# Kernel optimization log

Hardware: AMD Instinct MI355X
Metric: run time of the kernel (lower is better)

The kernel has to match this reference:

```python
import jax, jax.numpy as jnp
import numpy as np

NEG = -1000000000.0


def setup_inputs() -> dict:
    key = jax.random.key(0)
    k1, k2, k3, k4, k5 = jax.random.split(key, 5)
    B, T, D, Q = 8, 2048, 1024, 128
    x = jax.random.normal(k1, (B, T, D), dtype=jnp.float32)
    attn_mask = jax.random.randint(k2, (B, T), 0, 2).astype(jnp.bool_)
    s = 1.0 / np.sqrt(D)
    Wq = jax.random.normal(k3, (Q, D), dtype=jnp.float32) * s
    Wk = jax.random.normal(k4, (Q, D), dtype=jnp.float32) * s
    Wv = jax.random.normal(k5, (Q, D), dtype=jnp.float32) * s
    return {"x": x, "attn_mask": attn_mask, "Wq": Wq, "Wk": Wk, "Wv": Wv}


def reference(x, attn_mask, Wq, Wk, Wv):
    # x: (B,T,D); W*: (Q,D) torch Linear weights (y = x @ W.T)
    q = jnp.einsum('btd,qd->btq', x, Wq)
    k = jnp.einsum('btd,qd->btq', x, Wk)
    v = jnp.einsum('btd,qd->btq', x, Wv)
    logits = jnp.einsum('btq,bsq->bts', q, k)  # (B,T,T), no 1/sqrt(d) scaling (matches source)
    m = attn_mask[:, None, :]  # (B,1,T) broadcasts over query dim, == repeat(1,T,1)
    logits = jnp.where(m, logits, NEG)
    A = jax.nn.softmax(logits, axis=-1)
    A = jnp.where(m, A, 0.0)
    return jnp.einsum('bts,bsq->btq', A, v)
```

## Files before the change

kernel.cpp:

```cpp
#include <hip/hip_runtime.h>
#include <hip/hip_bf16.h>
#include <hip/hip_fp16.h>

typedef _Float16 half8 __attribute__((ext_vector_type(8)));
typedef _Float16 half4v __attribute__((ext_vector_type(4)));
typedef float float4v __attribute__((ext_vector_type(4)));

#define MFMA_F16(a, b, c) __builtin_amdgcn_mfma_f32_16x16x32_f16((a), (b), (c), 0, 0, 0)

#define GLDS16(gp, lp) \
    __builtin_amdgcn_global_load_lds((const __attribute__((address_space(1))) unsigned int*)(gp), \
                                     (__attribute__((address_space(3))) unsigned int*)(lp), 16, 0, 0)

#define BATCH 8
#define SEQ   2048
#define DIM   1024
#define QD    128
#define BT    (BATCH * SEQ)
#define NSPLIT 4
#define KSPAN (SEQ / NSPLIT)

__device__ __forceinline__ float dpp_max16(float x) {
    int v;
    v = __builtin_amdgcn_update_dpp(0, __float_as_int(x), 0xB1, 0xF, 0xF, false);
    x = fmaxf(x, __int_as_float(v));
    v = __builtin_amdgcn_update_dpp(0, __float_as_int(x), 0x4E, 0xF, 0xF, false);
    x = fmaxf(x, __int_as_float(v));
    v = __builtin_amdgcn_update_dpp(0, __float_as_int(x), 0x141, 0xF, 0xF, false);
    x = fmaxf(x, __int_as_float(v));
    v = __builtin_amdgcn_update_dpp(0, __float_as_int(x), 0x140, 0xF, 0xF, false);
    x = fmaxf(x, __int_as_float(v));
    return x;
}

__global__ __launch_bounds__(256) void cvt_x_kernel(const float* __restrict__ s,
                                                    _Float16* __restrict__ d) {
    int i = blockIdx.x * 256 + threadIdx.x;
    float4 f = ((const float4*)s)[i];
    half4v h = {(_Float16)f.x, (_Float16)f.y, (_Float16)f.z, (_Float16)f.w};
    ((half4v*)d)[i] = h;
}

__global__ __launch_bounds__(256) void cvt_w_kernel(const float* __restrict__ Wq,
                                                    const float* __restrict__ Wk,
                                                    const float* __restrict__ Wv,
                                                    _Float16* __restrict__ Wh) {
    const float* src = (blockIdx.y == 0) ? Wq : ((blockIdx.y == 1) ? Wk : Wv);
    int i = blockIdx.x * 256 + threadIdx.x;
    float4 f = ((const float4*)src)[i];
    half4v h = {(_Float16)f.x, (_Float16)f.y, (_Float16)f.z, (_Float16)f.w};
    ((half4v*)(Wh + (size_t)blockIdx.y * QD * DIM))[i] = h;
}

__global__ __launch_bounds__(256, 3) void proj_kernel(
    const _Float16* __restrict__ xh,
    const _Float16* __restrict__ Wh,
    _Float16* __restrict__ q_out,
    _Float16* __restrict__ k_out,
    _Float16* __restrict__ vt_out)
{
    __shared__ _Float16 As[64 * 64];
    __shared__ _Float16 Bs[128 * 64];

    const int tid  = threadIdx.x;
    const int lane = tid & 63;
    const int wave = tid >> 6;
    const int quad = lane >> 4;
    const int l15  = lane & 15;
    const int wr   = wave >> 1;
    const int wc   = wave & 1;

    const int which = blockIdx.y;
    const _Float16* W = Wh + (size_t)which * QD * DIM;
    const int row0 = blockIdx.x * 64;

    float4v acc[2][4];
#pragma unroll
    for (int rf = 0; rf < 2; rf++)
#pragma unroll
        for (int n = 0; n < 4; n++)
            acc[rf][n] = (float4v){0.f, 0.f, 0.f, 0.f};

    for (int kk = 0; kk < DIM; kk += 64) {
        __syncthreads();
#pragma unroll
        for (int c = 0; c < 2; c++) {
            int ci = wave * 128 + c * 64 + lane;
            int r  = ci >> 3;
            int g  = (ci & 7) ^ (r & 7);
            GLDS16(xh + (size_t)(row0 + r) * DIM + kk + g * 8, &As[(wave * 128 + c * 64) * 8]);
        }
#pragma unroll
        for (int c = 0; c < 4; c++) {
            int ci = wave * 256 + c * 64 + lane;
            int r  = ci >> 3;
            int g  = (ci & 7) ^ (r & 7);
            GLDS16(W + (size_t)r * DIM + kk + g * 8, &Bs[(wave * 256 + c * 64) * 8]);
        }
        __syncthreads();

        half8 af[2][2], bf[4][2];
#pragma unroll
        for (int rf = 0; rf < 2; rf++)
#pragma unroll
            for (int kc = 0; kc < 2; kc++) {
                int r = wr * 32 + rf * 16 + l15;
                int g = (kc * 4 + quad) ^ (r & 7);
                af[rf][kc] = *(const half8*)&As[r * 64 + g * 8];
            }
#pragma unroll
        for (int n = 0; n < 4; n++)
#pragma unroll
            for (int kc = 0; kc < 2; kc++) {
                int r = wc * 64 + n * 16 + l15;
                int g = (kc * 4 + quad) ^ (r & 7);
                bf[n][kc] = *(const half8*)&Bs[r * 64 + g * 8];
            }
#pragma unroll
        for (int kc = 0; kc < 2; kc++)
#pragma unroll
            for (int rf = 0; rf < 2; rf++)
#pragma unroll
                for (int n = 0; n < 4; n++)
                    acc[rf][n] = MFMA_F16(af[rf][kc], bf[n][kc], acc[rf][n]);
    }

    if (which == 2) {
#pragma unroll
        for (int rf = 0; rf < 2; rf++) {
            int grow0 = row0 + wr * 32 + rf * 16 + quad * 4;
            int b  = grow0 >> 11;
            int t0 = grow0 & 2047;
#pragma unroll
            for (int n = 0; n < 4; n++) {
                int col = wc * 64 + n * 16 + l15;
                half4v h;
#pragma unroll
                for (int r = 0; r < 4; r++) h[r] = (_Float16)acc[rf][n][r];
                *(half4v*)&vt_out[((size_t)(b * QD + col)) * SEQ + t0] = h;
            }
        }
    } else {
        _Float16* out = (which == 0) ? q_out : k_out;
#pragma unroll
        for (int rf = 0; rf < 2; rf++) {
            int grow0 = row0 + wr * 32 + rf * 16 + quad * 4;
#pragma unroll
            for (int n = 0; n < 4; n++) {
                int col = wc * 64 + n * 16 + l15;
#pragma unroll
                for (int r = 0; r < 4; r++)
                    out[(size_t)(grow0 + r) * QD + col] = (_Float16)acc[rf][n][r];
            }
        }
    }
}

__global__ __launch_bounds__(256, 2) void attn_kernel(
    const _Float16* __restrict__ q,
    const _Float16* __restrict__ k,
    const _Float16* __restrict__ vt,
    const int* __restrict__ mask,
    _Float16* __restrict__ Op,
    float2* __restrict__ ml)
{
    __shared__ _Float16 Ks[64 * 128];
    __shared__ _Float16 Vs[128 * 64];
    __shared__ _Float16 Ps[4 * 32 * 64];
    __shared__ int Ms[64];

    const int tid  = threadIdx.x;
    const int lane = tid & 63;
    const int wave = tid >> 6;
    const int quad = lane >> 4;
    const int l15  = lane & 15;

    const int b  = blockIdx.y;
    const int z  = blockIdx.z;
    const int rowbase = blockIdx.x * 128 + wave * 32;

    half8 qf[2][4];
#pragma unroll
    for (int rf = 0; rf < 2; rf++) {
        const _Float16* qrow = q + ((size_t)(b * SEQ + rowbase + rf * 16 + l15)) * QD + quad * 8;
#pragma unroll
        for (int kc = 0; kc < 4; kc++)
            qf[rf][kc] = *(const half8*)(qrow + kc * 32);
    }

    const half8 onesv = {(_Float16)1, (_Float16)1, (_Float16)1, (_Float16)1,
                         (_Float16)1, (_Float16)1, (_Float16)1, (_Float16)1};

    float4v oacc[2][8];
#pragma unroll
    for (int rf = 0; rf < 2; rf++)
#pragma unroll
        for (int n = 0; n < 8; n++)
            oacc[rf][n] = (float4v){0.f, 0.f, 0.f, 0.f};
    float4v lacc[2] = {(float4v){0.f, 0.f, 0.f, 0.f}, (float4v){0.f, 0.f, 0.f, 0.f}};
    float mrow[2][4];
#pragma unroll
    for (int rf = 0; rf < 2; rf++)
#pragma unroll
        for (int r = 0; r < 4; r++) mrow[rf][r] = -1e30f;

    _Float16* Pw = &Ps[wave * 32 * 64];

    for (int sb = z * KSPAN; sb < z * KSPAN + KSPAN; sb += 64) {
        __syncthreads();
#pragma unroll
        for (int c = 0; c < 4; c++) {
            int ci = wave * 256 + c * 64 + lane;
            int r  = ci >> 4;
            int gs = ci & 15;
            int g  = (gs & 8) | ((gs ^ r) & 7);
            GLDS16(k + ((size_t)(b * SEQ + sb + r)) * QD + g * 8, &Ks[(wave * 256 + c * 64) * 8]);
        }
#pragma unroll
        for (int c = 0; c < 4; c++) {
            int ci = wave * 256 + c * 64 + lane;
            int r  = ci >> 3;
            int g  = ((ci & 7) ^ r) & 7;
            GLDS16(vt + ((size_t)(b * QD + r)) * SEQ + sb + g * 8, &Vs[(wave * 256 + c * 64) * 8]);
        }
        if (tid < 64) Ms[tid] = mask[b * SEQ + sb + tid];
        __syncthreads();

        float4v sacc[2][4];
#pragma unroll
        for (int rf = 0; rf < 2; rf++)
#pragma unroll
            for (int j = 0; j < 4; j++)
                sacc[rf][j] = (float4v){0.f, 0.f, 0.f, 0.f};
#pragma unroll
        for (int kc = 0; kc < 4; kc++) {
            half8 kf[4];
#pragma unroll
            for (int j = 0; j < 4; j++) {
                int r  = j * 16 + l15;
                int g  = kc * 4 + quad;
                int gs = (g & 8) | ((g ^ r) & 7);
                kf[j] = *(const half8*)&Ks[r * 128 + gs * 8];
            }
#pragma unroll
            for (int rf = 0; rf < 2; rf++)
#pragma unroll
                for (int j = 0; j < 4; j++)
                    sacc[rf][j] = MFMA_F16(qf[rf][kc], kf[j], sacc[rf][j]);
        }

        float alpha[2][4];
#pragma unroll
        for (int rf = 0; rf < 2; rf++) {
            float rmax[4] = {-1e30f, -1e30f, -1e30f, -1e30f};
#pragma unroll
            for (int j = 0; j < 4; j++) {
                bool m_ok = (Ms[j * 16 + l15] != 0);
#pragma unroll
                for (int r = 0; r < 4; r++) {
                    float s = m_ok ? sacc[rf][j][r] : -1e30f;
                    sacc[rf][j][r] = s;
                    rmax[r] = fmaxf(rmax[r], s);
                }
            }
#pragma unroll
            for (int r = 0; r < 4; r++) {
                float rm = dpp_max16(rmax[r]);
                float mnew = fmaxf(mrow[rf][r], rm);
                alpha[rf][r] = __expf(mrow[rf][r] - mnew);
                mrow[rf][r] = mnew;
            }
        }

#pragma unroll
        for (int rf = 0; rf < 2; rf++)
#pragma unroll
            for (int j = 0; j < 4; j++) {
                int col = j * 16 + l15;
                int gc  = col >> 3;
#pragma unroll
                for (int r = 0; r < 4; r++) {
                    int m  = rf * 16 + quad * 4 + r;
                    int gs = (gc ^ m) & 7;
                    float s = sacc[rf][j][r];
                    float p = (s > -1e29f) ? __expf(s - mrow[rf][r]) : 0.f;
                    Pw[m * 64 + gs * 8 + (col & 7)] = (_Float16)p;
                }
            }

#pragma unroll
        for (int rf = 0; rf < 2; rf++) {
#pragma unroll
            for (int n = 0; n < 8; n++)
#pragma unroll
                for (int r = 0; r < 4; r++)
                    oacc[rf][n][r] *= alpha[rf][r];
#pragma unroll
            for (int r = 0; r < 4; r++) lacc[rf][r] *= alpha[rf][r];
        }

#pragma unroll
        for (int kc = 0; kc < 2; kc++) {
            half8 pf[2];
#pragma unroll
            for (int rf = 0; rf < 2; rf++) {
                int m  = rf * 16 + l15;
                int gs = ((kc * 4 + quad) ^ m) & 7;
                pf[rf] = *(const half8*)&Pw[m * 64 + gs * 8];
            }
#pragma unroll
            for (int n = 0; n < 8; n++) {
                int r  = n * 16 + l15;
                int gs = ((kc * 4 + quad) ^ r) & 7;
                half8 vf = *(const half8*)&Vs[r * 64 + gs * 8];
#pragma unroll
                for (int rf = 0; rf < 2; rf++)
                    oacc[rf][n] = MFMA_F16(pf[rf], vf, oacc[rf][n]);
            }
#pragma unroll
            for (int rf = 0; rf < 2; rf++)
                lacc[rf] = MFMA_F16(pf[rf], onesv, lacc[rf]);
        }
    }

    _Float16* Oz = Op + (size_t)z * BT * QD;
#pragma unroll
    for (int rf = 0; rf < 2; rf++) {
#pragma unroll
        for (int n = 0; n < 8; n++) {
            int col = n * 16 + l15;
#pragma unroll
            for (int r = 0; r < 4; r++) {
                int row = rowbase + rf * 16 + quad * 4 + r;
                Oz[((size_t)(b * SEQ + row)) * QD + col] = (_Float16)oacc[rf][n][r];
            }
        }
        if (l15 == 0) {
#pragma unroll
            for (int r = 0; r < 4; r++) {
                int row = rowbase + rf * 16 + quad * 4 + r;
                ml[(size_t)z * BT + b * SEQ + row] = make_float2(mrow[rf][r], lacc[rf][r]);
            }
        }
    }
}

__global__ __launch_bounds__(256) void merge_kernel(
    const _Float16* __restrict__ Op,
    const float2* __restrict__ ml,
    float* __restrict__ out)
{
    int gid = blockIdx.x * 256 + threadIdx.x;
    int row = gid >> 4;
    int c8  = (gid & 15) * 8;

    float2 a[NSPLIT];
    float m = -3.0e38f;
#pragma unroll
    for (int s = 0; s < NSPLIT; s++) { a[s] = ml[(size_t)s * BT + row]; m = fmaxf(m, a[s].x); }
    float sc[NSPLIT];
    float denom = 0.f;
#pragma unroll
    for (int s = 0; s < NSPLIT; s++) { sc[s] = __expf(a[s].x - m); denom += sc[s] * a[s].y; }
    float inv = (denom > 0.f) ? (1.0f / denom) : 0.f;

    float acc[8] = {0, 0, 0, 0, 0, 0, 0, 0};
#pragma unroll
    for (int s = 0; s < NSPLIT; s++) {
        half8 o = *(const half8*)&Op[(size_t)s * BT * QD + (size_t)row * QD + c8];
#pragma unroll
        for (int e = 0; e < 8; e++) acc[e] += (float)o[e] * sc[s];
    }
    float4 lo = make_float4(acc[0] * inv, acc[1] * inv, acc[2] * inv, acc[3] * inv);
    float4 hi = make_float4(acc[4] * inv, acc[5] * inv, acc[6] * inv, acc[7] * inv);
    *(float4*)&out[(size_t)row * QD + c8] = lo;
    *(float4*)&out[(size_t)row * QD + c8 + 4] = hi;
}

extern "C" void kernel_launch(void* const* d_in, const int* in_sizes, int n_in,
                              void* d_out, int out_size, void* d_ws, size_t ws_size,
                              hipStream_t stream) {
    const float* x    = (const float*)d_in[0];
    const int*   mask = (const int*)d_in[1];
    const float* Wq   = (const float*)d_in[2];
    const float* Wk   = (const float*)d_in[3];
    const float* Wv   = (const float*)d_in[4];
    float* out = (float*)d_out;

    char* p = (char*)d_ws;
    _Float16* xh  = (_Float16*)p; p += (size_t)BT * DIM * 2;
    _Float16* Wh  = (_Float16*)p; p += (size_t)3 * QD * DIM * 2;
    _Float16* qb  = (_Float16*)p; p += (size_t)BT * QD * 2;
    _Float16* kb  = (_Float16*)p; p += (size_t)BT * QD * 2;
    _Float16* vtb = (_Float16*)p; p += (size_t)BT * QD * 2;
    _Float16* Op  = (_Float16*)p; p += (size_t)NSPLIT * BT * QD * 2;
    float2*   ml  = (float2*)p;

    cvt_x_kernel<<<dim3(BT * DIM / 4 / 256), 256, 0, stream>>>(x, xh);
    cvt_w_kernel<<<dim3(QD * DIM / 4 / 256, 3), 256, 0, stream>>>(Wq, Wk, Wv, Wh);
    proj_kernel<<<dim3(BT / 64, 3), 256, 0, stream>>>(xh, Wh, qb, kb, vtb);
    attn_kernel<<<dim3(SEQ / 128, BATCH, NSPLIT), 256, 0, stream>>>(qb, kb, vtb, mask, Op, ml);
    merge_kernel<<<dim3(BT * 16 / 256), 256, 0, stream>>>(Op, ml, out);
}
```

Measured before the change: 163.4 us.

## Fuse convert kernels, widen projection K-tile, alias P onto K buffer, double splits

Merges the x and weight fp16 conversion kernels into one launch. Doubles the projection K-step to 128, halving the number of barrier-separated iterations. In attention, the P scratch now reuses the K tile's shared memory, with an added barrier, which cuts LDS use so launch bounds can request 4 blocks per SM. NSPLIT goes from 4 to 8 for more parallelism, at the cost of a larger partial-output buffer, more merge traffic and higher register pressure.

```diff
diff --git a/kernel.cpp b/kernel.cpp
--- a/kernel.cpp
+++ b/kernel.cpp
@@ -17,7 +17,7 @@
 #define DIM   1024
 #define QD    128
 #define BT    (BATCH * SEQ)
-#define NSPLIT 4
+#define NSPLIT 8
 #define KSPAN (SEQ / NSPLIT)
 
 __device__ __forceinline__ float dpp_max16(float x) {
@@ -33,23 +33,31 @@
     return x;
 }
 
-__global__ __launch_bounds__(256) void cvt_x_kernel(const float* __restrict__ s,
-                                                    _Float16* __restrict__ d) {
+#define XN4 (BT * DIM / 4)
+#define WN4 (3 * QD * DIM / 4)
+
+__global__ __launch_bounds__(256) void cvt_kernel(
+    const float* __restrict__ x,
+    const float* __restrict__ Wq,
+    const float* __restrict__ Wk,
+    const float* __restrict__ Wv,
+    _Float16* __restrict__ xh,
+    _Float16* __restrict__ Wh)
+{
     int i = blockIdx.x * 256 + threadIdx.x;
-    float4 f = ((const float4*)s)[i];
-    half4v h = {(_Float16)f.x, (_Float16)f.y, (_Float16)f.z, (_Float16)f.w};
-    ((half4v*)d)[i] = h;
-}
-
-__global__ __launch_bounds__(256) void cvt_w_kernel(const float* __restrict__ Wq,
-                                                    const float* __restrict__ Wk,
-                                                    const float* __restrict__ Wv,
-                                                    _Float16* __restrict__ Wh) {
-    const float* src = (blockIdx.y == 0) ? Wq : ((blockIdx.y == 1) ? Wk : Wv);
-    int i = blockIdx.x * 256 + threadIdx.x;
-    float4 f = ((const float4*)src)[i];
-    half4v h = {(_Float16)f.x, (_Float16)f.y, (_Float16)f.z, (_Float16)f.w};
-    ((half4v*)(Wh + (size_t)blockIdx.y * QD * DIM))[i] = h;
+    if (i < XN4) {
+        float4 f = ((const float4*)x)[i];
+        half4v h = {(_Float16)f.x, (_Float16)f.y, (_Float16)f.z, (_Float16)f.w};
+        ((half4v*)xh)[i] = h;
+    } else {
+        int j = i - XN4;
+        int which = j >> 15;
+        int o = j & 32767;
+        const float* src = (which == 0) ? Wq : ((which == 1) ? Wk : Wv);
+        float4 f = ((const float4*)src)[o];
+        half4v h = {(_Float16)f.x, (_Float16)f.y, (_Float16)f.z, (_Float16)f.w};
+        ((half4v*)Wh)[j] = h;
+    }
 }
 
 __global__ __launch_bounds__(256, 3) void proj_kernel(
@@ -59,8 +67,8 @@
     _Float16* __restrict__ k_out,
     _Float16* __restrict__ vt_out)
 {
-    __shared__ _Float16 As[64 * 64];
-    __shared__ _Float16 Bs[128 * 64];
+    __shared__ _Float16 As[64 * 128];
+    __shared__ _Float16 Bs[128 * 128];
 
     const int tid  = threadIdx.x;
     const int lane = tid & 63;
@@ -81,48 +89,49 @@
         for (int n = 0; n < 4; n++)
             acc[rf][n] = (float4v){0.f, 0.f, 0.f, 0.f};
 
-    for (int kk = 0; kk < DIM; kk += 64) {
+    for (int kk = 0; kk < DIM; kk += 128) {
         __syncthreads();
-#pragma unroll
-        for (int c = 0; c < 2; c++) {
-            int ci = wave * 128 + c * 64 + lane;
-            int r  = ci >> 3;
-            int g  = (ci & 7) ^ (r & 7);
-            GLDS16(xh + (size_t)(row0 + r) * DIM + kk + g * 8, &As[(wave * 128 + c * 64) * 8]);
-        }
 #pragma unroll
         for (int c = 0; c < 4; c++) {
             int ci = wave * 256 + c * 64 + lane;
-            int r  = ci >> 3;
-            int g  = (ci & 7) ^ (r & 7);
-            GLDS16(W + (size_t)r * DIM + kk + g * 8, &Bs[(wave * 256 + c * 64) * 8]);
+            int r  = ci >> 4;
+            int gs = ci & 15;
+            int g  = (gs & 8) | ((gs ^ r) & 7);
+            GLDS16(xh + (size_t)(row0 + r) * DIM + kk + g * 8, &As[(wave * 256 + c * 64) * 8]);
+        }
+#pragma unroll
+        for (int c = 0; c < 8; c++) {
+            int ci = wave * 512 + c * 64 + lane;
+            int r  = ci >> 4;
+            int gs = ci & 15;
+            int g  = (gs & 8) | ((gs ^ r) & 7);
+            GLDS16(W + (size_t)r * DIM + kk + g * 8, &Bs[(wave * 512 + c * 64) * 8]);
         }
         __syncthreads();
 
-        half8 af[2][2], bf[4][2];
-#pragma unroll
-        for (int rf = 0; rf < 2; rf++)
-#pragma unroll
-            for (int kc = 0; kc < 2; kc++) {
+#pragma unroll
+        for (int kc = 0; kc < 4; kc++) {
+            half8 af[2], bf[4];
+#pragma unroll
+            for (int rf = 0; rf < 2; rf++) {
                 int r = wr * 32 + rf * 16 + l15;
-                int g = (kc * 4 + quad) ^ (r & 7);
-                af[rf][kc] = *(const half8*)&As[r * 64 + g * 8];
-            }
-#pragma unroll
-        for (int n = 0; n < 4; n++)
-#pragma unroll
-            for (int kc = 0; kc < 2; kc++) {
+                int g = kc * 4 + quad;
+                int gp = (g & 8) | ((g ^ r) & 7);
+                af[rf] = *(const half8*)&As[r * 128 + gp * 8];
+            }
+#pragma unroll
+            for (int n = 0; n < 4; n++) {
                 int r = wc * 64 + n * 16 + l15;
-                int g = (kc * 4 + quad) ^ (r & 7);
-                bf[n][kc] = *(const half8*)&Bs[r * 64 + g * 8];
-            }
-#pragma unroll
-        for (int kc = 0; kc < 2; kc++)
+                int g = kc * 4 + quad;
+                int gp = (g & 8) | ((g ^ r) & 7);
+                bf[n] = *(const half8*)&Bs[r * 128 + gp * 8];
+            }
 #pragma unroll
             for (int rf = 0; rf < 2; rf++)
 #pragma unroll
                 for (int n = 0; n < 4; n++)
-                    acc[rf][n] = MFMA_F16(af[rf][kc], bf[n][kc], acc[rf][n]);
+                    acc[rf][n] = MFMA_F16(af[rf], bf[n], acc[rf][n]);
+        }
     }
 
     if (which == 2) {
@@ -156,7 +165,7 @@
     }
 }
 
-__global__ __launch_bounds__(256, 2) void attn_kernel(
+__global__ __launch_bounds__(256, 4) void attn_kernel(
     const _Float16* __restrict__ q,
     const _Float16* __restrict__ k,
     const _Float16* __restrict__ vt,
@@ -164,9 +173,8 @@
     _Float16* __restrict__ Op,
     float2* __restrict__ ml)
 {
-    __shared__ _Float16 Ks[64 * 128];
+    __shared__ _Float16 KPs[64 * 128];
     __shared__ _Float16 Vs[128 * 64];
-    __shared__ _Float16 Ps[4 * 32 * 64];
     __shared__ int Ms[64];
 
     const int tid  = threadIdx.x;
@@ -204,7 +212,7 @@
 #pragma unroll
         for (int r = 0; r < 4; r++) mrow[rf][r] = -1e30f;
 
-    _Float16* Pw = &Ps[wave * 32 * 64];
+    _Float16* Pw = &KPs[wave * 32 * 64];
 
     for (int sb = z * KSPAN; sb < z * KSPAN + KSPAN; sb += 64) {
         __syncthreads();
@@ -214,7 +222,7 @@
             int r  = ci >> 4;
             int gs = ci & 15;
             int g  = (gs & 8) | ((gs ^ r) & 7);
-            GLDS16(k + ((size_t)(b * SEQ + sb + r)) * QD + g * 8, &Ks[(wave * 256 + c * 64) * 8]);
+            GLDS16(k + ((size_t)(b * SEQ + sb + r)) * QD + g * 8, &KPs[(wave * 256 + c * 64) * 8]);
         }
 #pragma unroll
         for (int c = 0; c < 4; c++) {
@@ -240,7 +248,7 @@
                 int r  = j * 16 + l15;
                 int g  = kc * 4 + quad;
                 int gs = (g & 8) | ((g ^ r) & 7);
-                kf[j] = *(const half8*)&Ks[r * 128 + gs * 8];
+                kf[j] = *(const half8*)&KPs[r * 128 + gs * 8];
             }
 #pragma unroll
             for (int rf = 0; rf < 2; rf++)
@@ -271,6 +279,19 @@
                 mrow[rf][r] = mnew;
             }
         }
+
+#pragma unroll
+        for (int rf = 0; rf < 2; rf++) {
+#pragma unroll
+            for (int n = 0; n < 8; n++)
+#pragma unroll
+                for (int r = 0; r < 4; r++)
+                    oacc[rf][n][r] *= alpha[rf][r];
+#pragma unroll
+            for (int r = 0; r < 4; r++) lacc[rf][r] *= alpha[rf][r];
+        }
+
+        __syncthreads();
 
 #pragma unroll
         for (int rf = 0; rf < 2; rf++)
@@ -287,17 +308,6 @@
                     Pw[m * 64 + gs * 8 + (col & 7)] = (_Float16)p;
                 }
             }
-
-#pragma unroll
-        for (int rf = 0; rf < 2; rf++) {
-#pragma unroll
-            for (int n = 0; n < 8; n++)
-#pragma unroll
-                for (int r = 0; r < 4; r++)
-                    oacc[rf][n][r] *= alpha[rf][r];
-#pragma unroll
-            for (int r = 0; r < 4; r++) lacc[rf][r] *= alpha[rf][r];
-        }
 
 #pragma unroll
         for (int kc = 0; kc < 2; kc++) {
@@ -396,8 +406,7 @@
     _Float16* Op  = (_Float16*)p; p += (size_t)NSPLIT * BT * QD * 2;
     float2*   ml  = (float2*)p;
 
-    cvt_x_kernel<<<dim3(BT * DIM / 4 / 256), 256, 0, stream>>>(x, xh);
-    cvt_w_kernel<<<dim3(QD * DIM / 4 / 256, 3), 256, 0, stream>>>(Wq, Wk, Wv, Wh);
+    cvt_kernel<<<dim3((XN4 + WN4) / 256), 256, 0, stream>>>(x, Wq, Wk, Wv, xh, Wh);
     proj_kernel<<<dim3(BT / 64, 3), 256, 0, stream>>>(xh, Wh, qb, kb, vtb);
     attn_kernel<<<dim3(SEQ / 128, BATCH, NSPLIT), 256, 0, stream>>>(qb, kb, vtb, mask, Op, ml);
     merge_kernel<<<dim3(BT * 16 / 256), 256, 0, stream>>>(Op, ml, out);
```

Result: slower. 260.4 us (+59.4%).
